# Performance work log

Measured on AMD Instinct MI355X. Metric: run time of the kernel, lower is better.

## Reference

```python
import jax, jax.numpy as jnp
import numpy as np

NUM_HEADS = 16
THETA = 10000.0
EPS = 1e-5


def rmsnorm(x, g):
    ms = jnp.mean(x * x, axis=-1, keepdims=True)
    return x * jax.lax.rsqrt(ms + EPS) * g


def rope(x, positions, theta):
    # x: [b, h, s, dh]; rotate interleaved even/odd pairs
    dh = x.shape[-1]
    inv_freq = theta ** (-jnp.arange(0, dh, 2, dtype=jnp.float32) / dh)  # [dh/2]
    ang = positions.astype(jnp.float32)[:, None] * inv_freq[None, :]      # [s, dh/2]
    cos, sin = jnp.cos(ang), jnp.sin(ang)
    x1, x2 = x[..., 0::2], x[..., 1::2]
    r1 = x1 * cos - x2 * sin
    r2 = x1 * sin + x2 * cos
    return jnp.stack([r1, r2], axis=-1).reshape(x.shape)


def setup_inputs() -> dict:
    key = jax.random.key(0)
    ks = jax.random.split(key, 9)
    B, S, D, F = 2, 2048, 1024, 4096
    sd = 1.0 / np.sqrt(D)
    sf = 1.0 / np.sqrt(F)
    return {
        "x": jax.random.normal(ks[0], (B, S, D), dtype=jnp.float32),
        "wq": jax.random.normal(ks[1], (D, D), dtype=jnp.float32) * sd,
        "wk": jax.random.normal(ks[2], (D, D), dtype=jnp.float32) * sd,
        "wv": jax.random.normal(ks[3], (D, D), dtype=jnp.float32) * sd,
        "wo": jax.random.normal(ks[4], (D, D), dtype=jnp.float32) * sd,
        "w1": jax.random.normal(ks[5], (F, D), dtype=jnp.float32) * sd,
        "w2": jax.random.normal(ks[6], (D, F), dtype=jnp.float32) * sf,
        "w3": jax.random.normal(ks[7], (F, D), dtype=jnp.float32) * sd,
        "g1": jnp.ones((D,), dtype=jnp.float32),
        "g2": jnp.ones((D,), dtype=jnp.float32),
    }


def reference(x, wq, wk, wv, wo, w1, w2, w3, g1, g2):
    B, S, D = x.shape
    H = NUM_HEADS
    Dh = D // H
    pos = jnp.arange(S)

    # --- attention sublayer (pre-norm) ---
    h = rmsnorm(x, g1)
    # torch Linear weight is [out, in]: y = h @ w.T
    q = (h @ wq.T).reshape(B, S, H, Dh).transpose(0, 2, 1, 3)
    k = (h @ wk.T).reshape(B, S, H, Dh).transpose(0, 2, 1, 3)
    v = (h @ wv.T).reshape(B, S, H, Dh).transpose(0, 2, 1, 3)
    q = rope(q, pos, THETA)
    k = rope(k, pos, THETA)

    scores = jnp.einsum("bhqd,bhkd->bhqk", q, k) / jnp.sqrt(jnp.float32(Dh))
    causal = jnp.tril(jnp.ones((S, S), dtype=bool))
    scores = jnp.where(causal, scores, jnp.finfo(scores.dtype).min)
    attn = jax.nn.softmax(scores, axis=-1)
    o = jnp.einsum("bhqk,bhkd->bhqd", attn, v)
    o = o.transpose(0, 2, 1, 3).reshape(B, S, D) @ wo.T
    x = x + o

    # --- SwiGLU FFN sublayer (pre-norm) ---
    h2 = rmsnorm(x, g2)
    ff = (jax.nn.silu(h2 @ w1.T) * (h2 @ w3.T)) @ w2.T
    return x + ff
```

## Files before the change

kernel.cpp:

```cpp
#include <hip/hip_runtime.h>


typedef unsigned short u16;
typedef __attribute__((ext_vector_type(8))) short short8;
typedef __attribute__((ext_vector_type(4))) float f32x4;

#define MBYTE ((size_t)1 << 20)

typedef void __attribute__((address_space(3))) lds_void;
typedef void __attribute__((address_space(1))) glb_void;
#define GLD_LDS16(gp, lp) \
  __builtin_amdgcn_global_load_lds((glb_void*)(gp), (lds_void*)(lp), 16, 0, 0)

__device__ __forceinline__ u16 f2bf(float f) {
  union { float f; unsigned u; } v; v.f = f;
  unsigned r = v.u + 0x7FFFu + ((v.u >> 16) & 1u);
  return (u16)(r >> 16);
}
__device__ __forceinline__ float bf2f(u16 h) {
  union { unsigned u; float f; } v; v.u = ((unsigned)h) << 16;
  return v.f;
}

__global__ __launch_bounds__(256)
void prep_kernel(const float* __restrict__ wq, const float* __restrict__ wk,
                 const float* __restrict__ wv, const float* __restrict__ wo,
                 const float* __restrict__ w1, const float* __restrict__ w2,
                 const float* __restrict__ w3,
                 u16* wqb, u16* wkb, u16* wvb, u16* wob,
                 u16* w1b, u16* w2b, u16* w3b, float2* trig)
{
  const int y = blockIdx.y;
  if (y == 7) {
    const int idx = blockIdx.x * 256 + threadIdx.x;
    if (idx < 2048 * 32) {
      const int s = idx >> 5, i = idx & 31;
      const float inv = powf(10000.0f, -(float)(2 * i) / 64.0f);
      const float ang = (float)s * inv;
      trig[idx] = make_float2(cosf(ang), sinf(ang));
    }
    return;
  }
  const float* src; u16* dst; int n;
  switch (y) {
    case 0: src = wq; dst = wqb; n = 1 << 20; break;
    case 1: src = wk; dst = wkb; n = 1 << 20; break;
    case 2: src = wv; dst = wvb; n = 1 << 20; break;
    case 3: src = wo; dst = wob; n = 1 << 20; break;
    case 4: src = w1; dst = w1b; n = 1 << 22; break;
    case 5: src = w2; dst = w2b; n = 1 << 22; break;
    default: src = w3; dst = w3b; n = 1 << 22; break;
  }
  const int idx = (blockIdx.x * 256 + threadIdx.x) * 4;
  if (idx >= n) return;
  const float4 v = *(const float4*)(src + idx);
  ushort4 o; o.x = f2bf(v.x); o.y = f2bf(v.y); o.z = f2bf(v.z); o.w = f2bf(v.w);
  *(ushort4*)(dst + idx) = o;
}

__global__ __launch_bounds__(256)
void rmsnorm_kernel(const float* __restrict__ x, const float* __restrict__ g,
                    u16* __restrict__ out)
{
  __shared__ float red[4];
  const int row = blockIdx.x, tid = threadIdx.x;
  const float4 v = ((const float4*)(x + (size_t)row * 1024))[tid];
  float ss = v.x * v.x + v.y * v.y + v.z * v.z + v.w * v.w;
  #pragma unroll
  for (int off = 32; off >= 1; off >>= 1) ss += __shfl_xor(ss, off, 64);
  if ((tid & 63) == 0) red[tid >> 6] = ss;
  __syncthreads();
  const float tot = red[0] + red[1] + red[2] + red[3];
  const float rs = rsqrtf(tot * (1.0f / 1024.0f) + 1e-5f);
  const float4 gg = ((const float4*)g)[tid];
  ushort4 o;
  o.x = f2bf(v.x * rs * gg.x); o.y = f2bf(v.y * rs * gg.y);
  o.z = f2bf(v.z * rs * gg.z); o.w = f2bf(v.w * rs * gg.w);
  ((ushort4*)(out + (size_t)row * 1024))[tid] = o;
}

template<int TM, int TN, int WRN, int WCN>
__device__ __forceinline__ void gemm_core(const u16* __restrict__ A,
                                          const u16* __restrict__ Bw,
                                          int K, int bm, int bn,
                                          u16* As, u16* Bs,
                                          f32x4 (&acc)[TM / (16 * WRN)][TN / (16 * WCN)])
{
  constexpr int MT = TM / (16 * WRN), NT = TN / (16 * WCN);
  constexpr int CA = TM / 16, CB = TN / 16;
  const int tid = threadIdx.x, wid = tid >> 6, lane = tid & 63;
  const int wr = wid / WCN, wc = wid % WCN;
  const int lr = lane & 15, lg = lane >> 4;
  const int srow = lane >> 2;
  const int skel = (lane & 3) * 8;
  const size_t aRow0 = (size_t)bm * TM;
  const size_t bRow0 = (size_t)bn * TN;

  for (int k0 = 0; k0 < K; k0 += 32) {
    #pragma unroll
    for (int i = 0; i < CA / 4; i++) {
      int c = wid + i * 4;
      GLD_LDS16(A + (aRow0 + c * 16 + srow) * K + k0 + skel, As + c * 512);
    }
    #pragma unroll
    for (int i = 0; i < CB / 4; i++) {
      int c = wid + i * 4;
      GLD_LDS16(Bw + (bRow0 + c * 16 + srow) * K + k0 + skel, Bs + c * 512);
    }
    __syncthreads();
    short8 af[MT], bfr[NT];
    #pragma unroll
    for (int mt = 0; mt < MT; mt++)
      af[mt] = *(const short8*)&As[(wr * (MT * 16) + mt * 16 + lr) * 32 + lg * 8];
    #pragma unroll
    for (int nt = 0; nt < NT; nt++)
      bfr[nt] = *(const short8*)&Bs[(wc * (NT * 16) + nt * 16 + lr) * 32 + lg * 8];
    #pragma unroll
    for (int mt = 0; mt < MT; mt++)
      #pragma unroll
      for (int nt = 0; nt < NT; nt++)
        acc[mt][nt] = __builtin_amdgcn_mfma_f32_16x16x32_bf16(af[mt], bfr[nt],
                                                              acc[mt][nt], 0, 0, 0);
    __syncthreads();
  }
}

__global__ __launch_bounds__(256)
void gemm_qkv(const u16* __restrict__ A,
              const u16* __restrict__ wqb, const u16* __restrict__ wkb,
              const u16* __restrict__ wvb,
              u16* Qb, u16* Kb, u16* Vb, const float2* __restrict__ trig)
{
  __shared__ u16 As[128 * 32];
  __shared__ u16 Bs[128 * 32];
  const u16* Bw = blockIdx.z == 0 ? wqb : (blockIdx.z == 1 ? wkb : wvb);
  u16* out = blockIdx.z == 0 ? Qb : (blockIdx.z == 1 ? Kb : Vb);
  const bool isQK = blockIdx.z < 2;
  f32x4 acc[4][4];
  const f32x4 zero = {0.f, 0.f, 0.f, 0.f};
  #pragma unroll
  for (int i = 0; i < 4; i++)
    #pragma unroll
    for (int j = 0; j < 4; j++) acc[i][j] = zero;
  gemm_core<128, 128, 2, 2>(A, Bw, 1024, blockIdx.y, blockIdx.x, As, Bs, acc);
  const int lane = threadIdx.x & 63, wid = threadIdx.x >> 6;
  const int wr = wid >> 1, wc = wid & 1, lr = lane & 15, lg = lane >> 4;
  #pragma unroll
  for (int mt = 0; mt < 4; mt++)
    #pragma unroll
    for (int nt = 0; nt < 4; nt++)
      #pragma unroll
      for (int j = 0; j < 4; j++) {
        int row = blockIdx.y * 128 + wr * 64 + mt * 16 + lg * 4 + j;
        int col = blockIdx.x * 128 + wc * 64 + nt * 16 + lr;
        int b = row >> 11, s = row & 2047, hh = col >> 6, d = col & 63;
        float v = acc[mt][nt][j];
        if (isQK) {
          float p = __shfl_xor(v, 1);
          const float2 cs = trig[s * 32 + (d >> 1)];
          v = ((d & 1) == 0) ? (v * cs.x - p * cs.y)
                             : (p * cs.y + v * cs.x);
        }
        out[(((size_t)(b * 16 + hh)) * 2048 + s) * 64 + d] = f2bf(v);
      }
}

template<int EP, int TM, int TN, int WRN, int WCN>
__global__ __launch_bounds__(256)
void gemm_one(const u16* __restrict__ A, const u16* __restrict__ Bw, int K, int N,
              u16* outb, float* outf, const float* res, const u16* gatein)
{
  __shared__ u16 As[TM * 32];
  __shared__ u16 Bs[TN * 32];
  constexpr int MT = TM / (16 * WRN), NT = TN / (16 * WCN);
  f32x4 acc[MT][NT];
  const f32x4 zero = {0.f, 0.f, 0.f, 0.f};
  #pragma unroll
  for (int i = 0; i < MT; i++)
    #pragma unroll
    for (int j = 0; j < NT; j++) acc[i][j] = zero;
  gemm_core<TM, TN, WRN, WCN>(A, Bw, K, blockIdx.y, blockIdx.x, As, Bs, acc);
  const int lane = threadIdx.x & 63, wid = threadIdx.x >> 6;
  const int wr = wid / WCN, wc = wid % WCN, lr = lane & 15, lg = lane >> 4;
  #pragma unroll
  for (int mt = 0; mt < MT; mt++)
    #pragma unroll
    for (int nt = 0; nt < NT; nt++)
      #pragma unroll
      for (int j = 0; j < 4; j++) {
        int row = blockIdx.y * TM + wr * (MT * 16) + mt * 16 + lg * 4 + j;
        int col = blockIdx.x * TN + wc * (NT * 16) + nt * 16 + lr;
        size_t o = (size_t)row * N + col;
        float v = acc[mt][nt][j];
        if constexpr (EP == 1) {
          outb[o] = f2bf(v);
        } else if constexpr (EP == 2) {
          outf[o] = res[o] + v;
        } else {
          float a1 = bf2f(gatein[o]);
          float sg = a1 / (1.0f + __expf(-a1));
          outb[o] = f2bf(sg * v);
        }
      }
}

__global__ __launch_bounds__(256)
void flash_attn(const u16* __restrict__ Qb, const u16* __restrict__ Kb,
                const u16* __restrict__ Vb, u16* __restrict__ Ob)
{
  __shared__ u16 Ks[64 * 64];
  __shared__ u16 Vt[64 * 64];
  __shared__ u16 Ps[4 * 16 * 72];
  const int tid = threadIdx.x, wid = tid >> 6, lane = tid & 63;
  const int lr = lane & 15, lg = lane >> 4;
  const int qt = blockIdx.x, bh = blockIdx.y;
  const size_t base = (size_t)bh * (2048 * 64);

  short8 qf[2];
  #pragma unroll
  for (int kc = 0; kc < 2; kc++)
    qf[kc] = *(const short8*)&Qb[base + (size_t)(qt * 64 + wid * 16 + lr) * 64
                                 + kc * 32 + lg * 8];

  f32x4 oacc[4];
  float mrow[4], lrow[4];
  const f32x4 zero = {0.f, 0.f, 0.f, 0.f};
  #pragma unroll
  for (int d = 0; d < 4; d++) oacc[d] = zero;
  #pragma unroll
  for (int j = 0; j < 4; j++) { mrow[j] = -1e30f; lrow[j] = 0.0f; }

  for (int kt = 0; kt <= qt; kt++) {
    #pragma unroll
    for (int c = 0; c < 2; c++) {
      int ci = (wid * 2 + c) * 64 + lane;
      int row = ci >> 3;
      int lch = (ci & 7) ^ (row & 7);
      GLD_LDS16(Kb + base + (size_t)(kt * 64 + row) * 64 + lch * 8,
                (u16*)Ks + (wid * 2 + c) * 512);
    }
    #pragma unroll
    for (int c = 0; c < 2; c++) {
      int key = lane;
      int dc = c * 4 + wid;
      short8 vv = *(const short8*)&Vb[base + (size_t)(kt * 64 + key) * 64 + dc * 8];
      #pragma unroll
      for (int j = 0; j < 8; j++) {
        int d = dc * 8 + j;
        int byt = d * 128 + (((key >> 3) ^ (d & 7)) << 4) + ((key & 7) << 1);
        *(u16*)((char*)Vt + byt) = (u16)vv[j];
      }
    }
    __syncthreads();

    f32x4 sv[4];
    #pragma unroll
    for (int nt = 0; nt < 4; nt++) {
      f32x4 s = zero;
      #pragma unroll
      for (int kc = 0; kc < 2; kc++) {
        int row = nt * 16 + lr;
        int pch = (kc * 4 + lg) ^ (row & 7);
        short8 kf = *(const short8*)((const char*)Ks + row * 128 + pch * 16);
        s = __builtin_amdgcn_mfma_f32_16x16x32_bf16(qf[kc], kf, s, 0, 0, 0);
      }
      s *= 0.125f;
      if (kt == qt) {
        int key = kt * 64 + nt * 16 + lr;
        #pragma unroll
        for (int j = 0; j < 4; j++) {
          int q = qt * 64 + wid * 16 + lg * 4 + j;
          if (key > q) s[j] = -1e30f;
        }
      }
      sv[nt] = s;
    }

    #pragma unroll
    for (int j = 0; j < 4; j++) {
      float tm = fmaxf(fmaxf(sv[0][j], sv[1][j]), fmaxf(sv[2][j], sv[3][j]));
      #pragma unroll
      for (int off = 8; off >= 1; off >>= 1) tm = fmaxf(tm, __shfl_xor(tm, off, 64));
      float mnew = fmaxf(mrow[j], tm);
      float esc = __expf(mrow[j] - mnew);
      mrow[j] = mnew;
      float rs = 0.f;
      #pragma unroll
      for (int nt = 0; nt < 4; nt++) {
        float p = __expf(sv[nt][j] - mnew);
        sv[nt][j] = p;
        rs += p;
      }
      #pragma unroll
      for (int off = 8; off >= 1; off >>= 1) rs += __shfl_xor(rs, off, 64);
      lrow[j] = lrow[j] * esc + rs;
      #pragma unroll
      for (int dt = 0; dt < 4; dt++) oacc[dt][j] *= esc;
    }

    u16* myP = (u16*)Ps + wid * (16 * 72);
    #pragma unroll
    for (int nt = 0; nt < 4; nt++)
      #pragma unroll
      for (int j = 0; j < 4; j++)
        myP[(lg * 4 + j) * 72 + nt * 16 + lr] = f2bf(sv[nt][j]);
    asm volatile("s_waitcnt lgkmcnt(0)" ::: "memory");
    short8 pa[2];
    #pragma unroll
    for (int kc = 0; kc < 2; kc++)
      pa[kc] = *(const short8*)&myP[lr * 72 + kc * 32 + lg * 8];

    #pragma unroll
    for (int dt = 0; dt < 4; dt++) {
      #pragma unroll
      for (int kc = 0; kc < 2; kc++) {
        int d = dt * 16 + lr;
        int pch = (kc * 4 + lg) ^ (d & 7);
        short8 vf = *(const short8*)((const char*)Vt + d * 128 + pch * 16);
        oacc[dt] = __builtin_amdgcn_mfma_f32_16x16x32_bf16(pa[kc], vf, oacc[dt], 0, 0, 0);
      }
    }
    __syncthreads();
  }

  const int b = bh >> 4, h = bh & 15;
  #pragma unroll
  for (int dt = 0; dt < 4; dt++)
    #pragma unroll
    for (int j = 0; j < 4; j++) {
      int sq = qt * 64 + wid * 16 + lg * 4 + j;
      Ob[((size_t)(b * 2048 + sq)) * 1024 + h * 64 + dt * 16 + lr] =
          f2bf(oacc[dt][j] / lrow[j]);
    }
}

extern "C" void kernel_launch(void* const* d_in, const int* in_sizes, int n_in,
                              void* d_out, int out_size, void* d_ws, size_t ws_size,
                              hipStream_t stream)
{
  const float* x  = (const float*)d_in[0];
  const float* wq = (const float*)d_in[1];
  const float* wk = (const float*)d_in[2];
  const float* wv = (const float*)d_in[3];
  const float* wo = (const float*)d_in[4];
  const float* w1 = (const float*)d_in[5];
  const float* w2 = (const float*)d_in[6];
  const float* w3 = (const float*)d_in[7];
  const float* g1 = (const float*)d_in[8];
  const float* g2 = (const float*)d_in[9];
  float* out = (float*)d_out;
  char* ws = (char*)d_ws;

  u16*    wqb  = (u16*)   (ws + 0 * MBYTE);
  u16*    wkb  = (u16*)   (ws + 2 * MBYTE);
  u16*    wvb  = (u16*)   (ws + 4 * MBYTE);
  u16*    wob  = (u16*)   (ws + 6 * MBYTE);
  u16*    w1b  = (u16*)   (ws + 8 * MBYTE);
  u16*    w2b  = (u16*)   (ws + 16 * MBYTE);
  u16*    w3b  = (u16*)   (ws + 24 * MBYTE);
  float2* trig = (float2*)(ws + 32 * MBYTE);
  float*  x2   = (float*) (ws + 33 * MBYTE);
  u16*    hb   = (u16*)   (ws + 49 * MBYTE);
  u16*    Qb   = (u16*)   (ws + 57 * MBYTE);
  u16*    Kb   = (u16*)   (ws + 65 * MBYTE);
  u16*    Vb   = (u16*)   (ws + 73 * MBYTE);
  u16*    Ob   = (u16*)   (ws + 81 * MBYTE);
  u16*    f1   = (u16*)   (ws + 57 * MBYTE);

  prep_kernel<<<dim3(4096, 8), 256, 0, stream>>>(wq, wk, wv, wo, w1, w2, w3,
                                                 wqb, wkb, wvb, wob, w1b, w2b, w3b,
                                                 trig);
  rmsnorm_kernel<<<4096, 256, 0, stream>>>(x, g1, hb);
  gemm_qkv<<<dim3(8, 32, 3), 256, 0, stream>>>(hb, wqb, wkb, wvb, Qb, Kb, Vb, trig);
  flash_attn<<<dim3(32, 32), 256, 0, stream>>>(Qb, Kb, Vb, Ob);
  gemm_one<2, 64, 128, 1, 4><<<dim3(8, 64), 256, 0, stream>>>(
      Ob, wob, 1024, 1024, nullptr, x2, x, nullptr);
  rmsnorm_kernel<<<4096, 256, 0, stream>>>(x2, g2, hb);
  gemm_one<1, 128, 128, 2, 2><<<dim3(32, 32), 256, 0, stream>>>(
      hb, w1b, 1024, 4096, f1, nullptr, nullptr, nullptr);
  gemm_one<3, 128, 128, 2, 2><<<dim3(32, 32), 256, 0, stream>>>(
      hb, w3b, 1024, 4096, f1, nullptr, nullptr, f1);
  gemm_one<2, 64, 128, 1, 4><<<dim3(8, 64), 256, 0, stream>>>(
      f1, w2b, 4096, 1024, nullptr, out, x2, nullptr);
}
```

Baseline: 573.2 us.

## Fuse W1/W3 FFN GEMMs with SwiGLU epilogue; double-buffer flash attention K/V

Measured after the change: 497.8 us. -13.2%, faster.

```diff
diff --git a/kernel.cpp b/kernel.cpp
--- a/kernel.cpp
+++ b/kernel.cpp
@@ -168,7 +168,7 @@
 template<int EP, int TM, int TN, int WRN, int WCN>
 __global__ __launch_bounds__(256)
 void gemm_one(const u16* __restrict__ A, const u16* __restrict__ Bw, int K, int N,
-              u16* outb, float* outf, const float* res, const u16* gatein)
+              u16* outb, float* outf, const float* res)
 {
   __shared__ u16 As[TM * 32];
   __shared__ u16 Bs[TN * 32];
@@ -194,13 +194,73 @@
         float v = acc[mt][nt][j];
         if constexpr (EP == 1) {
           outb[o] = f2bf(v);
-        } else if constexpr (EP == 2) {
+        } else {
           outf[o] = res[o] + v;
-        } else {
-          float a1 = bf2f(gatein[o]);
-          float sg = a1 / (1.0f + __expf(-a1));
-          outb[o] = f2bf(sg * v);
         }
+      }
+}
+
+__global__ __launch_bounds__(256)
+void gemm_ffn13(const u16* __restrict__ A, const u16* __restrict__ W1,
+                const u16* __restrict__ W3, u16* __restrict__ outb)
+{
+  __shared__ u16 As[128 * 32];
+  __shared__ u16 B1s[64 * 32];
+  __shared__ u16 B3s[64 * 32];
+  f32x4 acc1[4][2], acc3[4][2];
+  const f32x4 zero = {0.f, 0.f, 0.f, 0.f};
+  #pragma unroll
+  for (int i = 0; i < 4; i++)
+    #pragma unroll
+    for (int j = 0; j < 2; j++) { acc1[i][j] = zero; acc3[i][j] = zero; }
+  const int tid = threadIdx.x, wid = tid >> 6, lane = tid & 63;
+  const int wr = wid >> 1, wc = wid & 1;
+  const int lr = lane & 15, lg = lane >> 4;
+  const int srow = lane >> 2;
+  const int skel = (lane & 3) * 8;
+  const size_t aRow0 = (size_t)blockIdx.y * 128;
+  const size_t bRow0 = (size_t)blockIdx.x * 64;
+
+  for (int k0 = 0; k0 < 1024; k0 += 32) {
+    #pragma unroll
+    for (int i = 0; i < 2; i++) {
+      int c = wid + i * 4;
+      GLD_LDS16(A + (aRow0 + c * 16 + srow) * 1024 + k0 + skel, As + c * 512);
+    }
+    GLD_LDS16(W1 + (bRow0 + wid * 16 + srow) * 1024 + k0 + skel, B1s + wid * 512);
+    GLD_LDS16(W3 + (bRow0 + wid * 16 + srow) * 1024 + k0 + skel, B3s + wid * 512);
+    __syncthreads();
+    short8 af[4], b1[2], b3[2];
+    #pragma unroll
+    for (int mt = 0; mt < 4; mt++)
+      af[mt] = *(const short8*)&As[(wr * 64 + mt * 16 + lr) * 32 + lg * 8];
+    #pragma unroll
+    for (int nt = 0; nt < 2; nt++) {
+      b1[nt] = *(const short8*)&B1s[(wc * 32 + nt * 16 + lr) * 32 + lg * 8];
+      b3[nt] = *(const short8*)&B3s[(wc * 32 + nt * 16 + lr) * 32 + lg * 8];
+    }
+    #pragma unroll
+    for (int mt = 0; mt < 4; mt++)
+      #pragma unroll
+      for (int nt = 0; nt < 2; nt++) {
+        acc1[mt][nt] = __builtin_amdgcn_mfma_f32_16x16x32_bf16(af[mt], b1[nt],
+                                                               acc1[mt][nt], 0, 0, 0);
+        acc3[mt][nt] = __builtin_amdgcn_mfma_f32_16x16x32_bf16(af[mt], b3[nt],
+                                                               acc3[mt][nt], 0, 0, 0);
+      }
+    __syncthreads();
+  }
+  #pragma unroll
+  for (int mt = 0; mt < 4; mt++)
+    #pragma unroll
+    for (int nt = 0; nt < 2; nt++)
+      #pragma unroll
+      for (int j = 0; j < 4; j++) {
+        int row = blockIdx.y * 128 + wr * 64 + mt * 16 + lg * 4 + j;
+        int col = blockIdx.x * 64 + wc * 32 + nt * 16 + lr;
+        float v1 = acc1[mt][nt][j], v3 = acc3[mt][nt][j];
+        float sg = v1 / (1.0f + __expf(-v1));
+        outb[(size_t)row * 4096 + col] = f2bf(sg * v3);
       }
 }
 
@@ -208,12 +268,13 @@
 void flash_attn(const u16* __restrict__ Qb, const u16* __restrict__ Kb,
                 const u16* __restrict__ Vb, u16* __restrict__ Ob)
 {
-  __shared__ u16 Ks[64 * 64];
-  __shared__ u16 Vt[64 * 64];
+  __shared__ u16 Ks[2][64 * 64];
+  __shared__ u16 Vt[2][64 * 64];
   __shared__ u16 Ps[4 * 16 * 72];
   const int tid = threadIdx.x, wid = tid >> 6, lane = tid & 63;
   const int lr = lane & 15, lg = lane >> 4;
-  const int qt = blockIdx.x, bh = blockIdx.y;
+  const int bh = blockIdx.y;
+  const int qt = (blockIdx.x + blockIdx.y) & 31;
   const size_t base = (size_t)bh * (2048 * 64);
 
   short8 qf[2];
@@ -230,28 +291,44 @@
   #pragma unroll
   for (int j = 0; j < 4; j++) { mrow[j] = -1e30f; lrow[j] = 0.0f; }
 
+  short8 vv[2];
+  #pragma unroll
+  for (int c = 0; c < 2; c++) {
+    int ci = (wid * 2 + c) * 64 + lane;
+    int row = ci >> 3;
+    int lch = (ci & 7) ^ (row & 7);
+    GLD_LDS16(Kb + base + (size_t)(row)*64 + lch * 8, (u16*)Ks[0] + (wid * 2 + c) * 512);
+  }
+  #pragma unroll
+  for (int c = 0; c < 2; c++)
+    vv[c] = *(const short8*)&Vb[base + (size_t)lane * 64 + (c * 4 + wid) * 8];
+  asm volatile("s_waitcnt vmcnt(0)" ::: "memory");
+  #pragma unroll
+  for (int c = 0; c < 2; c++)
+    #pragma unroll
+    for (int j = 0; j < 8; j++) {
+      int d = (c * 4 + wid) * 8 + j;
+      int byt = d * 128 + (((lane >> 3) ^ (d & 7)) << 4) + ((lane & 7) << 1);
+      *(u16*)((char*)Vt[0] + byt) = (u16)vv[c][j];
+    }
+  __syncthreads();
+
+  int buf = 0;
   for (int kt = 0; kt <= qt; kt++) {
-    #pragma unroll
-    for (int c = 0; c < 2; c++) {
-      int ci = (wid * 2 + c) * 64 + lane;
-      int row = ci >> 3;
-      int lch = (ci & 7) ^ (row & 7);
-      GLD_LDS16(Kb + base + (size_t)(kt * 64 + row) * 64 + lch * 8,
-                (u16*)Ks + (wid * 2 + c) * 512);
-    }
-    #pragma unroll
-    for (int c = 0; c < 2; c++) {
-      int key = lane;
-      int dc = c * 4 + wid;
-      short8 vv = *(const short8*)&Vb[base + (size_t)(kt * 64 + key) * 64 + dc * 8];
-      #pragma unroll
-      for (int j = 0; j < 8; j++) {
-        int d = dc * 8 + j;
-        int byt = d * 128 + (((key >> 3) ^ (d & 7)) << 4) + ((key & 7) << 1);
-        *(u16*)((char*)Vt + byt) = (u16)vv[j];
-      }
-    }
-    __syncthreads();
+    if (kt < qt) {
+      #pragma unroll
+      for (int c = 0; c < 2; c++) {
+        int ci = (wid * 2 + c) * 64 + lane;
+        int row = ci >> 3;
+        int lch = (ci & 7) ^ (row & 7);
+        GLD_LDS16(Kb + base + (size_t)((kt + 1) * 64 + row) * 64 + lch * 8,
+                  (u16*)Ks[buf ^ 1] + (wid * 2 + c) * 512);
+      }
+      #pragma unroll
+      for (int c = 0; c < 2; c++)
+        vv[c] = *(const short8*)&Vb[base + (size_t)((kt + 1) * 64 + lane) * 64
+                                    + (c * 4 + wid) * 8];
+    }
 
     f32x4 sv[4];
     #pragma unroll
@@ -261,7 +338,7 @@
       for (int kc = 0; kc < 2; kc++) {
         int row = nt * 16 + lr;
         int pch = (kc * 4 + lg) ^ (row & 7);
-        short8 kf = *(const short8*)((const char*)Ks + row * 128 + pch * 16);
+        short8 kf = *(const short8*)((const char*)Ks[buf] + row * 128 + pch * 16);
         s = __builtin_amdgcn_mfma_f32_16x16x32_bf16(qf[kc], kf, s, 0, 0, 0);
       }
       s *= 0.125f;
@@ -316,11 +393,24 @@
       for (int kc = 0; kc < 2; kc++) {
         int d = dt * 16 + lr;
         int pch = (kc * 4 + lg) ^ (d & 7);
-        short8 vf = *(const short8*)((const char*)Vt + d * 128 + pch * 16);
+        short8 vf = *(const short8*)((const char*)Vt[buf] + d * 128 + pch * 16);
         oacc[dt] = __builtin_amdgcn_mfma_f32_16x16x32_bf16(pa[kc], vf, oacc[dt], 0, 0, 0);
       }
     }
+
+    if (kt < qt) {
+      asm volatile("s_waitcnt vmcnt(0)" ::: "memory");
+      #pragma unroll
+      for (int c = 0; c < 2; c++)
+        #pragma unroll
+        for (int j = 0; j < 8; j++) {
+          int d = (c * 4 + wid) * 8 + j;
+          int byt = d * 128 + (((lane >> 3) ^ (d & 7)) << 4) + ((lane & 7) << 1);
+          *(u16*)((char*)Vt[buf ^ 1] + byt) = (u16)vv[c][j];
+        }
+    }
     __syncthreads();
+    buf ^= 1;
   }
 
   const int b = bh >> 4, h = bh & 15;
@@ -374,12 +464,9 @@
   gemm_qkv<<<dim3(8, 32, 3), 256, 0, stream>>>(hb, wqb, wkb, wvb, Qb, Kb, Vb, trig);
   flash_attn<<<dim3(32, 32), 256, 0, stream>>>(Qb, Kb, Vb, Ob);
   gemm_one<2, 64, 128, 1, 4><<<dim3(8, 64), 256, 0, stream>>>(
-      Ob, wob, 1024, 1024, nullptr, x2, x, nullptr);
+      Ob, wob, 1024, 1024, nullptr, x2, x);
   rmsnorm_kernel<<<4096, 256, 0, stream>>>(x2, g2, hb);
-  gemm_one<1, 128, 128, 2, 2><<<dim3(32, 32), 256, 0, stream>>>(
-      hb, w1b, 1024, 4096, f1, nullptr, nullptr, nullptr);
-  gemm_one<3, 128, 128, 2, 2><<<dim3(32, 32), 256, 0, stream>>>(
-      hb, w3b, 1024, 4096, f1, nullptr, nullptr, f1);
+  gemm_ffn13<<<dim3(64, 32), 256, 0, stream>>>(hb, w1b, w3b, f1);
   gemm_one<2, 64, 128, 1, 4><<<dim3(8, 64), 256, 0, stream>>>(
-      f1, w2b, 4096, 1024, nullptr, out, x2, nullptr);
-}
+      f1, w2b, 4096, 1024, nullptr, out, x2);
+}
```
